# Kernel optimization log

Hardware: AMD Instinct MI355X
Metric: run time of the kernel (lower is better)

The kernel has to match this reference:

```python
import jax, jax.numpy as jnp
import numpy as np

N_NODES = 50000


def _segment_softmax(alpha, dst, num_segments):
    # alpha: [E, H] edge attention logits, softmax-normalized per destination node
    m = jax.ops.segment_max(alpha, dst, num_segments=num_segments)
    m = jnp.where(jnp.isfinite(m), m, 0.0)
    e = jnp.exp(alpha - m[dst])
    s = jax.ops.segment_sum(e, dst, num_segments=num_segments)
    return e / (s[dst] + 1e-16)


def _gat_layer(x, W, att_src, att_dst, bias, src, dst, heads, ch, concat):
    N = x.shape[0]
    xp = (x @ W).reshape(N, heads, ch)                      # [N, H, C]
    a_s = jnp.einsum('nhc,hc->nh', xp, att_src)              # [N, H]
    a_d = jnp.einsum('nhc,hc->nh', xp, att_dst)              # [N, H]
    alpha = jax.nn.leaky_relu(a_s[src] + a_d[dst], 0.2)      # [E, H]
    alpha = _segment_softmax(alpha, dst, N)
    out = jax.ops.segment_sum(alpha[:, :, None] * xp[src], dst, num_segments=N)  # [N, H, C]
    out = out.reshape(N, heads * ch) if concat else out.mean(axis=1)
    return out + bias


def setup_inputs() -> dict:
    key = jax.random.key(0)
    ks = jax.random.split(key, 10)
    IN, HID, HEADS, OUT, E = 128, 64, 4, 32, 640000
    x = jax.random.normal(ks[0], (N_NODES, IN), jnp.float32)
    edge_index = jax.random.randint(ks[1], (2, E), 0, N_NODES, dtype=jnp.int32)
    W1 = jax.random.normal(ks[2], (IN, HEADS * HID), jnp.float32) * (1.0 / np.sqrt(IN))
    att_src1 = jax.random.normal(ks[3], (HEADS, HID), jnp.float32) * 0.1
    att_dst1 = jax.random.normal(ks[4], (HEADS, HID), jnp.float32) * 0.1
    b1 = jnp.zeros((HEADS * HID,), jnp.float32)
    W2 = jax.random.normal(ks[5], (HEADS * HID, OUT), jnp.float32) * (1.0 / np.sqrt(HEADS * HID))
    att_src2 = jax.random.normal(ks[6], (1, OUT), jnp.float32) * 0.1
    att_dst2 = jax.random.normal(ks[7], (1, OUT), jnp.float32) * 0.1
    b2 = jnp.zeros((OUT,), jnp.float32)
    return {"x": x, "edge_index": edge_index, "W1": W1, "att_src1": att_src1,
            "att_dst1": att_dst1, "b1": b1, "W2": W2, "att_src2": att_src2,
            "att_dst2": att_dst2, "b2": b2}


def reference(x, edge_index, W1, att_src1, att_dst1, b1, W2, att_src2, att_dst2, b2):
    N = x.shape[0]
    # PyG GATConv default: add self-loops
    loop = jnp.arange(N, dtype=edge_index.dtype)
    src = jnp.concatenate([edge_index[0], loop])
    dst = jnp.concatenate([edge_index[1], loop])
    HID = att_src1.shape[1]
    HEADS = att_src1.shape[0]
    OUT = att_src2.shape[1]
    # dropout layers are identity in eval mode
    h = jax.nn.elu(_gat_layer(x, W1, att_src1, att_dst1, b1, src, dst, HEADS, HID, True))
    out = _gat_layer(h, W2, att_src2, att_dst2, b2, src, dst, 1, OUT, False)
    return jax.nn.softmax(out, axis=1)
```

## Files before the change

### kernel.cpp

```cpp
#include <hip/hip_runtime.h>
#include <math.h>
#include <stdint.h>

#define NEG_SENT -1e30f

typedef __attribute__((ext_vector_type(8))) short bf16x8;
typedef __attribute__((ext_vector_type(4))) float f32x4;

__device__ __forceinline__ unsigned short f2bf(float f) {
    unsigned u = __float_as_uint(f);
    unsigned r = u + 0x7FFFu + ((u >> 16) & 1u);
    return (unsigned short)(r >> 16);
}
__device__ __forceinline__ float bf2f(unsigned short h) {
    return __uint_as_float(((unsigned)h) << 16);
}

__global__ __launch_bounds__(256) void prep_count(const float* __restrict__ w1,
        const float* __restrict__ w2, unsigned short* __restrict__ w1t,
        unsigned short* __restrict__ w2t, const int* __restrict__ ei,
        int E, int Etot, int* __restrict__ deg) {
    int b = blockIdx.x;
    if (b < 160) {
        int tidx = b * 256 + threadIdx.x;
        if (b < 128) {
            int k = tidx & 127, n = tidx >> 7;
            w1t[tidx] = f2bf(w1[k * 256 + n]);
        } else {
            int idx = tidx - 32768;
            int k = idx & 255, n = idx >> 8;
            w2t[idx] = f2bf(w2[k * 32 + n]);
        }
    } else {
        int e = (b - 160) * 256 + threadIdx.x;
        if (e >= Etot) return;
        int d = (e < E) ? ei[E + e] : e - E;
        atomicAdd(&deg[d], 1);
    }
}

__global__ __launch_bounds__(256) void gemm1_mfma(
        const float* __restrict__ x,
        const unsigned short* __restrict__ w1t,
        const float* __restrict__ att_s, const float* __restrict__ att_d,
        unsigned short* __restrict__ xph,
        float* __restrict__ a_s, float* __restrict__ a_d, int M) {
    int wave = (int)(((long)blockIdx.x * 256 + threadIdx.x) >> 6);
    int lane = threadIdx.x & 63;
    int row0 = wave * 16;
    if (row0 >= M) return;
    int r = lane & 15;
    int g = lane >> 4;
    bf16x8 a[4];
    const float* arow = x + (long)(row0 + r) * 128 + g * 8;
    #pragma unroll
    for (int k0 = 0; k0 < 4; ++k0) {
        float4 f0 = *(const float4*)(arow + k0 * 32);
        float4 f1 = *(const float4*)(arow + k0 * 32 + 4);
        bf16x8 af;
        af[0] = (short)f2bf(f0.x); af[1] = (short)f2bf(f0.y);
        af[2] = (short)f2bf(f0.z); af[3] = (short)f2bf(f0.w);
        af[4] = (short)f2bf(f1.x); af[5] = (short)f2bf(f1.y);
        af[6] = (short)f2bf(f1.z); af[7] = (short)f2bf(f1.w);
        a[k0] = af;
    }
    float as_v[16], ad_v[16];
    #pragma unroll
    for (int nt = 0; nt < 16; ++nt) {
        as_v[nt] = att_s[nt * 16 + r];
        ad_v[nt] = att_d[nt * 16 + r];
    }
    f32x4 acc[16];
    #pragma unroll
    for (int nt = 0; nt < 16; ++nt) acc[nt] = (f32x4){0.f, 0.f, 0.f, 0.f};
    #pragma unroll
    for (int nt = 0; nt < 16; ++nt) {
        const unsigned short* brow = w1t + (long)(nt * 16 + r) * 128 + g * 8;
        #pragma unroll
        for (int k0 = 0; k0 < 4; ++k0) {
            bf16x8 b = *(const bf16x8*)(brow + k0 * 32);
            acc[nt] = __builtin_amdgcn_mfma_f32_16x16x32_bf16(a[k0], b, acc[nt], 0, 0, 0);
        }
    }
    float ps[4][4] = {};
    float pd[4][4] = {};
    #pragma unroll
    for (int nt = 0; nt < 16; ++nt) {
        int hh = nt >> 2;
        #pragma unroll
        for (int q = 0; q < 4; ++q) {
            float v = acc[nt][q];
            xph[(long)(row0 + g * 4 + q) * 256 + nt * 16 + r] = f2bf(v);
            ps[q][hh] += v * as_v[nt];
            pd[q][hh] += v * ad_v[nt];
        }
    }
    #pragma unroll
    for (int off = 1; off < 16; off <<= 1) {
        #pragma unroll
        for (int q = 0; q < 4; ++q)
            #pragma unroll
            for (int hh = 0; hh < 4; ++hh) {
                ps[q][hh] += __shfl_xor(ps[q][hh], off);
                pd[q][hh] += __shfl_xor(pd[q][hh], off);
            }
    }
    if (r == 0) {
        #pragma unroll
        for (int q = 0; q < 4; ++q) {
            int row = row0 + g * 4 + q;
            #pragma unroll
            for (int hh = 0; hh < 4; ++hh) {
                a_s[row * 4 + hh] = ps[q][hh];
                a_d[row * 4 + hh] = pd[q][hh];
            }
        }
    }
}

__global__ __launch_bounds__(256) void gemm2_mfma(
        const unsigned short* __restrict__ hb,
        const unsigned short* __restrict__ w2t,
        const float* __restrict__ att_s, const float* __restrict__ att_d,
        unsigned short* __restrict__ xp2h,
        float* __restrict__ a_s, float* __restrict__ a_d, int M) {
    int wave = (int)(((long)blockIdx.x * 256 + threadIdx.x) >> 6);
    int lane = threadIdx.x & 63;
    int row0 = wave * 16;
    if (row0 >= M) return;
    int r = lane & 15;
    int g = lane >> 4;
    bf16x8 a[8];
    const unsigned short* arow = hb + (long)(row0 + r) * 256 + g * 8;
    #pragma unroll
    for (int k0 = 0; k0 < 8; ++k0)
        a[k0] = *(const bf16x8*)(arow + k0 * 32);
    float as_v[2], ad_v[2];
    #pragma unroll
    for (int nt = 0; nt < 2; ++nt) {
        as_v[nt] = att_s[nt * 16 + r];
        ad_v[nt] = att_d[nt * 16 + r];
    }
    f32x4 acc[2];
    acc[0] = (f32x4){0.f, 0.f, 0.f, 0.f};
    acc[1] = (f32x4){0.f, 0.f, 0.f, 0.f};
    #pragma unroll
    for (int nt = 0; nt < 2; ++nt) {
        const unsigned short* brow = w2t + (long)(nt * 16 + r) * 256 + g * 8;
        #pragma unroll
        for (int k0 = 0; k0 < 8; ++k0) {
            bf16x8 b = *(const bf16x8*)(brow + k0 * 32);
            acc[nt] = __builtin_amdgcn_mfma_f32_16x16x32_bf16(a[k0], b, acc[nt], 0, 0, 0);
        }
    }
    float ps[4] = {}, pd[4] = {};
    #pragma unroll
    for (int nt = 0; nt < 2; ++nt) {
        #pragma unroll
        for (int q = 0; q < 4; ++q) {
            float v = acc[nt][q];
            xp2h[(long)(row0 + g * 4 + q) * 32 + nt * 16 + r] = f2bf(v);
            ps[q] += v * as_v[nt];
            pd[q] += v * ad_v[nt];
        }
    }
    #pragma unroll
    for (int off = 1; off < 16; off <<= 1) {
        #pragma unroll
        for (int q = 0; q < 4; ++q) {
            ps[q] += __shfl_xor(ps[q], off);
            pd[q] += __shfl_xor(pd[q], off);
        }
    }
    if (r == 0) {
        #pragma unroll
        for (int q = 0; q < 4; ++q) {
            a_s[row0 + g * 4 + q] = ps[q];
            a_d[row0 + g * 4 + q] = pd[q];
        }
    }
}

__global__ __launch_bounds__(256) void scan_local(const int* __restrict__ deg,
        int* __restrict__ rowptr, int* __restrict__ blocksum, int N) {
    __shared__ int part[256];
    int b = blockIdx.x, t = threadIdx.x;
    int base = b * 1024 + t * 4;
    int4 v = make_int4(0, 0, 0, 0);
    if (base + 3 < N) {
        v = *(const int4*)(deg + base);
    } else {
        if (base + 0 < N) v.x = deg[base + 0];
        if (base + 1 < N) v.y = deg[base + 1];
        if (base + 2 < N) v.z = deg[base + 2];
        if (base + 3 < N) v.w = deg[base + 3];
    }
    part[t] = v.x + v.y + v.z + v.w;
    __syncthreads();
    #pragma unroll
    for (int off = 1; off < 256; off <<= 1) {
        int val = (t >= off) ? part[t - off] : 0;
        __syncthreads();
        part[t] += val;
        __syncthreads();
    }
    if (t == 255) blocksum[b] = part[255];
    int r0 = (t > 0) ? part[t - 1] : 0;
    int r1 = r0 + v.x;
    int r2 = r1 + v.y;
    int r3 = r2 + v.z;
    if (base + 3 < N) {
        *(int4*)(rowptr + base) = make_int4(r0, r1, r2, r3);
    } else {
        if (base + 0 < N) rowptr[base + 0] = r0;
        if (base + 1 < N) rowptr[base + 1] = r1;
        if (base + 2 < N) rowptr[base + 2] = r2;
        if (base + 3 < N) rowptr[base + 3] = r3;
    }
}

__global__ __launch_bounds__(256) void scan_add(int* __restrict__ rowptr,
        const int* __restrict__ blocksum, int* __restrict__ cursor,
        int N, int Etot, int nb) {
    __shared__ int part[256];
    int b = blockIdx.x, t = threadIdx.x;
    part[t] = (t < nb) ? blocksum[t] : 0;
    __syncthreads();
    #pragma unroll
    for (int off = 1; off < 256; off <<= 1) {
        int val = (t >= off) ? part[t - off] : 0;
        __syncthreads();
        part[t] += val;
        __syncthreads();
    }
    int off_b = (b > 0) ? part[b - 1] : 0;
    int base = b * 1024 + t * 4;
    if (base + 3 < N) {
        int4 v = *(const int4*)(rowptr + base);
        v.x += off_b; v.y += off_b; v.z += off_b; v.w += off_b;
        *(int4*)(rowptr + base) = v;
        *(int4*)(cursor + base) = v;
    } else {
        for (int i = 0; i < 4; ++i) {
            if (base + i < N) {
                int v = rowptr[base + i] + off_b;
                rowptr[base + i] = v;
                cursor[base + i] = v;
            }
        }
    }
    if (b == 0 && t == 0) rowptr[N] = Etot;
}

__global__ __launch_bounds__(256) void scatter_edges(const int* __restrict__ ei,
        int E, int Etot, int* __restrict__ cursor, int* __restrict__ csr_src) {
    int e = blockIdx.x * 256 + threadIdx.x;
    if (e >= Etot) return;
    int s, d;
    if (e < E) { s = ei[e]; d = ei[E + e]; } else { s = e - E; d = s; }
    int pos = atomicAdd(&cursor[d], 1);
    csr_src[pos] = s;
}

__global__ __launch_bounds__(256) void sort_rows(const int* __restrict__ rowptr,
        int* __restrict__ csr_src, int N) {
    __shared__ int buf[4][256];
    int t = threadIdx.x;
    int w = t >> 6;
    int lane = t & 63;
    int d = blockIdx.x * 4 + w;
    if (d >= N) return;
    int row0 = rowptr[d];
    int deg = rowptr[d + 1] - row0;
    if (deg <= 64) {
        int v = (lane < deg) ? csr_src[row0 + lane] : 0x7FFFFFFF;
        #pragma unroll
        for (int k = 2; k <= 64; k <<= 1) {
            for (int jj = k >> 1; jj > 0; jj >>= 1) {
                int u = __shfl_xor(v, jj);
                bool up = ((lane & k) == 0);
                bool lower = ((lane & jj) == 0);
                int mn = min(v, u), mx = max(v, u);
                v = (up == lower) ? mn : mx;
            }
        }
        if (lane < deg) csr_src[row0 + lane] = v;
    } else if (deg <= 256) {
        for (int j = lane; j < deg; j += 64) buf[w][j] = csr_src[row0 + j];
        for (int it = 0; it < deg; ++it) {
            int start = it & 1;
            #pragma unroll
            for (int rep = 0; rep < 2; ++rep) {
                int k = start + 2 * lane + rep * 128;
                if (k + 1 < deg) {
                    int a = buf[w][k], b = buf[w][k + 1];
                    if (a > b) { buf[w][k] = b; buf[w][k + 1] = a; }
                }
            }
        }
        for (int j = lane; j < deg; j += 64) csr_src[row0 + j] = buf[w][j];
    } else if (lane == 0) {
        for (int i = 1; i < deg; ++i) {
            int key = csr_src[row0 + i];
            int k = i - 1;
            while (k >= 0 && csr_src[row0 + k] > key) {
                csr_src[row0 + k + 1] = csr_src[row0 + k];
                --k;
            }
            csr_src[row0 + k + 1] = key;
        }
    }
}

__global__ __launch_bounds__(256) void agg1_fused(const int* __restrict__ rowptr,
        const int* __restrict__ csr_src, const float* __restrict__ a_s,
        const float* __restrict__ a_d, const ushort4* __restrict__ xph4,
        const float* __restrict__ bias, ushort4* __restrict__ hb4, int N) {
    __shared__ unsigned short cbuf[4][1024];
    int t = threadIdx.x;
    int w = t >> 6;
    int lane = t & 63;
    int d = blockIdx.x * 4 + w;
    bool active = d < N;
    int row0 = 0, deg = 0;
    if (active) { row0 = rowptr[d]; deg = rowptr[d + 1] - row0; }
    int h = lane & 3;
    int j0 = lane >> 2;
    float ad = active ? a_d[d * 4 + h] : 0.f;
    float mraw = NEG_SENT;
    for (int j = j0; j < deg; j += 16) {
        int sn = csr_src[row0 + j];
        mraw = fmaxf(mraw, a_s[sn * 4 + h]);
    }
    #pragma unroll
    for (int off = 4; off <= 32; off <<= 1) mraw = fmaxf(mraw, __shfl_xor(mraw, off));
    float m = mraw + ad;
    m = m > 0.f ? m : 0.2f * m;
    float s = 0.f;
    for (int j = j0; j < deg; j += 16) {
        int sn = csr_src[row0 + j];
        float l = a_s[sn * 4 + h] + ad;
        l = l > 0.f ? l : 0.2f * l;
        float e = expf(l - m);
        if (j < 256) cbuf[w][j * 4 + h] = f2bf(e);
        s += e;
    }
    #pragma unroll
    for (int off = 4; off <= 32; off <<= 1) s += __shfl_xor(s, off);
    float inv = 1.f / (s + 1e-16f);
    if (!active) return;
    int hsel = lane >> 4;
    float m_h   = __shfl(m, hsel);
    float inv_h = __shfl(inv, hsel);
    float ad_h  = __shfl(ad, hsel);
    int cap = deg < 256 ? deg : 256;
    float4 acc = make_float4(0.f, 0.f, 0.f, 0.f);
    int j = 0;
    for (; j + 4 <= cap; j += 4) {
        long e0 = row0 + j;
        int s0 = csr_src[e0 + 0];
        int s1 = csr_src[e0 + 1];
        int s2 = csr_src[e0 + 2];
        int s3 = csr_src[e0 + 3];
        float c0 = bf2f(cbuf[w][(j + 0) * 4 + hsel]);
        float c1 = bf2f(cbuf[w][(j + 1) * 4 + hsel]);
        float c2 = bf2f(cbuf[w][(j + 2) * 4 + hsel]);
        float c3 = bf2f(cbuf[w][(j + 3) * 4 + hsel]);
        ushort4 u0 = xph4[(long)s0 * 64 + lane];
        ushort4 u1 = xph4[(long)s1 * 64 + lane];
        ushort4 u2 = xph4[(long)s2 * 64 + lane];
        ushort4 u3 = xph4[(long)s3 * 64 + lane];
        acc.x += c0 * bf2f(u0.x); acc.y += c0 * bf2f(u0.y);
        acc.z += c0 * bf2f(u0.z); acc.w += c0 * bf2f(u0.w);
        acc.x += c1 * bf2f(u1.x); acc.y += c1 * bf2f(u1.y);
        acc.z += c1 * bf2f(u1.z); acc.w += c1 * bf2f(u1.w);
        acc.x += c2 * bf2f(u2.x); acc.y += c2 * bf2f(u2.y);
        acc.z += c2 * bf2f(u2.z); acc.w += c2 * bf2f(u2.w);
        acc.x += c3 * bf2f(u3.x); acc.y += c3 * bf2f(u3.y);
        acc.z += c3 * bf2f(u3.z); acc.w += c3 * bf2f(u3.w);
    }
    for (; j < deg; ++j) {
        long e = row0 + j;
        int sn = csr_src[e];
        float c;
        if (j < 256) {
            c = bf2f(cbuf[w][j * 4 + hsel]);
        } else {
            float l = a_s[sn * 4 + hsel] + ad_h;
            l = l > 0.f ? l : 0.2f * l;
            c = bf2f(f2bf(expf(l - m_h)));
        }
        ushort4 u = xph4[(long)sn * 64 + lane];
        acc.x += c * bf2f(u.x); acc.y += c * bf2f(u.y);
        acc.z += c * bf2f(u.z); acc.w += c * bf2f(u.w);
    }
    float4 b = ((const float4*)bias)[lane];
    float vx = acc.x * inv_h + b.x; vx = vx > 0.f ? vx : expm1f(vx);
    float vy = acc.y * inv_h + b.y; vy = vy > 0.f ? vy : expm1f(vy);
    float vz = acc.z * inv_h + b.z; vz = vz > 0.f ? vz : expm1f(vz);
    float vw = acc.w * inv_h + b.w; vw = vw > 0.f ? vw : expm1f(vw);
    ushort4 o;
    o.x = f2bf(vx); o.y = f2bf(vy); o.z = f2bf(vz); o.w = f2bf(vw);
    hb4[(long)d * 64 + lane] = o;
}

__global__ __launch_bounds__(256) void agg2_fused(const int* __restrict__ rowptr,
        const int* __restrict__ csr_src, const float* __restrict__ a_s,
        const float* __restrict__ a_d, const unsigned short* __restrict__ xp2h,
        const float* __restrict__ bias, float* __restrict__ out, int N) {
    __shared__ unsigned short ebuf[8][256];
    int t = threadIdx.x;
    int w2 = t >> 5;
    int d = blockIdx.x * 8 + w2;
    if (d >= N) return;
    int c = t & 31;
    int row0 = rowptr[d];
    int deg = rowptr[d + 1] - row0;
    float ad = a_d[d];
    float mraw = NEG_SENT;
    for (int j = c; j < deg; j += 32) {
        int sn = csr_src[row0 + j];
        mraw = fmaxf(mraw, a_s[sn]);
    }
    #pragma unroll
    for (int off = 1; off <= 16; off <<= 1) mraw = fmaxf(mraw, __shfl_xor(mraw, off, 32));
    float m = mraw + ad;
    m = m > 0.f ? m : 0.2f * m;
    float s = 0.f;
    for (int j = c; j < deg; j += 32) {
        int sn = csr_src[row0 + j];
        float l = a_s[sn] + ad;
        l = l > 0.f ? l : 0.2f * l;
        float e = expf(l - m);
        if (j < 256) ebuf[w2][j] = f2bf(e);
        s += e;
    }
    #pragma unroll
    for (int off = 1; off <= 16; off <<= 1) s += __shfl_xor(s, off, 32);
    float inv = 1.f / (s + 1e-16f);
    int cap = deg < 256 ? deg : 256;
    float acc = 0.f;
    int j = 0;
    for (; j + 4 <= cap; j += 4) {
        long e0 = row0 + j;
        int s0 = csr_src[e0 + 0];
        int s1 = csr_src[e0 + 1];
        int s2 = csr_src[e0 + 2];
        int s3 = csr_src[e0 + 3];
        float c0 = bf2f(ebuf[w2][j + 0]);
        float c1 = bf2f(ebuf[w2][j + 1]);
        float c2 = bf2f(ebuf[w2][j + 2]);
        float c3 = bf2f(ebuf[w2][j + 3]);
        float v0 = bf2f(xp2h[(long)s0 * 32 + c]);
        float v1 = bf2f(xp2h[(long)s1 * 32 + c]);
        float v2 = bf2f(xp2h[(long)s2 * 32 + c]);
        float v3 = bf2f(xp2h[(long)s3 * 32 + c]);
        acc += c0 * v0;
        acc += c1 * v1;
        acc += c2 * v2;
        acc += c3 * v3;
    }
    for (; j < deg; ++j) {
        long e = row0 + j;
        int sn = csr_src[e];
        float co;
        if (j < 256) {
            co = bf2f(ebuf[w2][j]);
        } else {
            float l = a_s[sn] + ad; l = l > 0.f ? l : 0.2f * l;
            co = bf2f(f2bf(expf(l - m)));
        }
        acc += co * bf2f(xp2h[(long)sn * 32 + c]);
    }
    float v = acc * inv + bias[c];
    float mx = v;
    #pragma unroll
    for (int off = 16; off; off >>= 1) mx = fmaxf(mx, __shfl_xor(mx, off, 32));
    float ex = expf(v - mx);
    float sm = ex;
    #pragma unroll
    for (int off = 16; off; off >>= 1) sm += __shfl_xor(sm, off, 32);
    out[(long)d * 32 + c] = ex / sm;
}

extern "C" void kernel_launch(void* const* d_in, const int* in_sizes, int n_in,
                              void* d_out, int out_size, void* d_ws, size_t ws_size,
                              hipStream_t stream) {
    const float* x   = (const float*)d_in[0];
    const int*   ei  = (const int*)d_in[1];
    const float* W1  = (const float*)d_in[2];
    const float* as1 = (const float*)d_in[3];
    const float* ad1 = (const float*)d_in[4];
    const float* b1  = (const float*)d_in[5];
    const float* W2  = (const float*)d_in[6];
    const float* as2 = (const float*)d_in[7];
    const float* ad2 = (const float*)d_in[8];
    const float* b2  = (const float*)d_in[9];
    float* out = (float*)d_out;

    const int N = in_sizes[0] / 128;
    const int E = in_sizes[1] / 2;
    const int Etot = E + N;

    unsigned short* xp1h = (unsigned short*)d_ws;
    unsigned short* hb   = xp1h + (long)N * 256;
    unsigned short* w1t  = hb + (long)N * 256;
    unsigned short* w2t  = w1t + 32768;
    unsigned short* xp2h = w2t + 8192;
    float* a_s1   = (float*)(xp2h + (long)N * 32);
    float* a_d1   = a_s1 + (long)N * 4;
    float* a_s2   = a_d1 + (long)N * 4;
    float* a_d2   = a_s2 + N;
    int* deg      = (int*)(a_d2 + N);
    int* rowptr   = deg + N;
    int* cursor   = rowptr + N + 4;
    int* csr_src  = cursor + N;
    int* blocksum = csr_src + Etot;

    hipMemsetAsync(deg, 0, (size_t)N * sizeof(int), stream);

    int nbE = (Etot + 255) / 256;
    int nbS = (N + 1023) / 1024;
    prep_count<<<160 + nbE, 256, 0, stream>>>(W1, W2, w1t, w2t, ei, E, Etot, deg);
    scan_local<<<nbS, 256, 0, stream>>>(deg, rowptr, blocksum, N);
    scan_add<<<nbS, 256, 0, stream>>>(rowptr, blocksum, cursor, N, Etot, nbS);
    scatter_edges<<<nbE, 256, 0, stream>>>(ei, E, Etot, cursor, csr_src);
    sort_rows<<<(N + 3) / 4, 256, 0, stream>>>(rowptr, csr_src, N);

    int gemmBlocks = (((N + 15) / 16) + 3) / 4;

    gemm1_mfma<<<gemmBlocks, 256, 0, stream>>>(x, w1t, as1, ad1,
                                               xp1h, a_s1, a_d1, N);
    agg1_fused<<<(N + 3) / 4, 256, 0, stream>>>(rowptr, csr_src, a_s1, a_d1,
                                                (const ushort4*)xp1h, b1,
                                                (ushort4*)hb, N);

    gemm2_mfma<<<gemmBlocks, 256, 0, stream>>>(hb, w2t, as2, ad2,
                                               xp2h, a_s2, a_d2, N);
    agg2_fused<<<(N + 7) / 8, 256, 0, stream>>>(rowptr, csr_src, a_s2, a_d2,
                                                xp2h, b2, out, N);
}
```

Measured before the change: 235.3 us.

## Fuse per-row CSR sort into layer-1 aggregation and reuse sorted indices from registers

Removes the separate sort_rows kernel and sorts each destination row at the start of agg1_fused. The sorted result is still written back for agg2. For rows with degree up to 64, the sorted source indices stay in registers and are read with lane shuffles instead of being reloaded from global memory. This saves a launch and a full pass over csr_src, in exchange for a longer, more register-heavy aggregation kernel; an unused merge_ms helper is also added.

```diff
diff --git a/kernel.cpp b/kernel.cpp
--- a/kernel.cpp
+++ b/kernel.cpp
@@ -262,9 +262,18 @@
     csr_src[pos] = s;
 }
 
-__global__ __launch_bounds__(256) void sort_rows(const int* __restrict__ rowptr,
-        int* __restrict__ csr_src, int N) {
-    __shared__ int buf[4][256];
+__device__ __forceinline__ void merge_ms(float& m, float& s, float m2, float s2) {
+    float mn = fmaxf(m, m2);
+    s = s * expf(m - mn) + s2 * expf(m2 - mn);
+    m = mn;
+}
+
+__global__ __launch_bounds__(256) void agg1_fused(const int* __restrict__ rowptr,
+        int* __restrict__ csr_src, const float* __restrict__ a_s,
+        const float* __restrict__ a_d, const ushort4* __restrict__ xph4,
+        const float* __restrict__ bias, ushort4* __restrict__ hb4, int N) {
+    __shared__ int shmem[4][512];
+    unsigned short (*cbuf)[1024] = (unsigned short (*)[1024])shmem;
     int t = threadIdx.x;
     int w = t >> 6;
     int lane = t & 63;
@@ -272,33 +281,36 @@
     if (d >= N) return;
     int row0 = rowptr[d];
     int deg = rowptr[d + 1] - row0;
-    if (deg <= 64) {
-        int v = (lane < deg) ? csr_src[row0 + lane] : 0x7FFFFFFF;
+
+    int sv = 0x7FFFFFFF;
+    bool reg_sorted = (deg <= 64);
+    if (reg_sorted) {
+        if (lane < deg) sv = csr_src[row0 + lane];
         #pragma unroll
         for (int k = 2; k <= 64; k <<= 1) {
             for (int jj = k >> 1; jj > 0; jj >>= 1) {
-                int u = __shfl_xor(v, jj);
+                int u = __shfl_xor(sv, jj);
                 bool up = ((lane & k) == 0);
                 bool lower = ((lane & jj) == 0);
-                int mn = min(v, u), mx = max(v, u);
-                v = (up == lower) ? mn : mx;
+                int mn = min(sv, u), mx = max(sv, u);
+                sv = (up == lower) ? mn : mx;
             }
         }
-        if (lane < deg) csr_src[row0 + lane] = v;
+        if (lane < deg) csr_src[row0 + lane] = sv;
     } else if (deg <= 256) {
-        for (int j = lane; j < deg; j += 64) buf[w][j] = csr_src[row0 + j];
+        for (int j = lane; j < deg; j += 64) shmem[w][j] = csr_src[row0 + j];
         for (int it = 0; it < deg; ++it) {
             int start = it & 1;
             #pragma unroll
             for (int rep = 0; rep < 2; ++rep) {
                 int k = start + 2 * lane + rep * 128;
                 if (k + 1 < deg) {
-                    int a = buf[w][k], b = buf[w][k + 1];
-                    if (a > b) { buf[w][k] = b; buf[w][k + 1] = a; }
+                    int a = shmem[w][k], b = shmem[w][k + 1];
+                    if (a > b) { shmem[w][k] = b; shmem[w][k + 1] = a; }
                 }
             }
         }
-        for (int j = lane; j < deg; j += 64) csr_src[row0 + j] = buf[w][j];
+        for (int j = lane; j < deg; j += 64) csr_src[row0 + j] = shmem[w][j];
     } else if (lane == 0) {
         for (int i = 1; i < deg; ++i) {
             int key = csr_src[row0 + i];
@@ -310,45 +322,38 @@
             csr_src[row0 + k + 1] = key;
         }
     }
-}
-
-__global__ __launch_bounds__(256) void agg1_fused(const int* __restrict__ rowptr,
-        const int* __restrict__ csr_src, const float* __restrict__ a_s,
-        const float* __restrict__ a_d, const ushort4* __restrict__ xph4,
-        const float* __restrict__ bias, ushort4* __restrict__ hb4, int N) {
-    __shared__ unsigned short cbuf[4][1024];
-    int t = threadIdx.x;
-    int w = t >> 6;
-    int lane = t & 63;
-    int d = blockIdx.x * 4 + w;
-    bool active = d < N;
-    int row0 = 0, deg = 0;
-    if (active) { row0 = rowptr[d]; deg = rowptr[d + 1] - row0; }
+
     int h = lane & 3;
     int j0 = lane >> 2;
-    float ad = active ? a_d[d * 4 + h] : 0.f;
+    float ad = a_d[d * 4 + h];
+    int iters = (deg + 15) >> 4;
     float mraw = NEG_SENT;
-    for (int j = j0; j < deg; j += 16) {
-        int sn = csr_src[row0 + j];
-        mraw = fmaxf(mraw, a_s[sn * 4 + h]);
+    for (int it = 0; it < iters; ++it) {
+        int j = j0 + (it << 4);
+        int jc = (j < deg) ? j : 0;
+        int sn = reg_sorted ? __shfl(sv, jc) : csr_src[row0 + jc];
+        if (j < deg) mraw = fmaxf(mraw, a_s[sn * 4 + h]);
     }
     #pragma unroll
     for (int off = 4; off <= 32; off <<= 1) mraw = fmaxf(mraw, __shfl_xor(mraw, off));
     float m = mraw + ad;
     m = m > 0.f ? m : 0.2f * m;
     float s = 0.f;
-    for (int j = j0; j < deg; j += 16) {
-        int sn = csr_src[row0 + j];
-        float l = a_s[sn * 4 + h] + ad;
-        l = l > 0.f ? l : 0.2f * l;
-        float e = expf(l - m);
-        if (j < 256) cbuf[w][j * 4 + h] = f2bf(e);
-        s += e;
+    for (int it = 0; it < iters; ++it) {
+        int j = j0 + (it << 4);
+        int jc = (j < deg) ? j : 0;
+        int sn = reg_sorted ? __shfl(sv, jc) : csr_src[row0 + jc];
+        if (j < deg) {
+            float l = a_s[sn * 4 + h] + ad;
+            l = l > 0.f ? l : 0.2f * l;
+            float e = expf(l - m);
+            if (j < 256) cbuf[w][j * 4 + h] = f2bf(e);
+            s += e;
+        }
     }
     #pragma unroll
     for (int off = 4; off <= 32; off <<= 1) s += __shfl_xor(s, off);
     float inv = 1.f / (s + 1e-16f);
-    if (!active) return;
     int hsel = lane >> 4;
     float m_h   = __shfl(m, hsel);
     float inv_h = __shfl(inv, hsel);
@@ -357,11 +362,10 @@
     float4 acc = make_float4(0.f, 0.f, 0.f, 0.f);
     int j = 0;
     for (; j + 4 <= cap; j += 4) {
-        long e0 = row0 + j;
-        int s0 = csr_src[e0 + 0];
-        int s1 = csr_src[e0 + 1];
-        int s2 = csr_src[e0 + 2];
-        int s3 = csr_src[e0 + 3];
+        int s0 = reg_sorted ? __shfl(sv, j + 0) : csr_src[row0 + j + 0];
+        int s1 = reg_sorted ? __shfl(sv, j + 1) : csr_src[row0 + j + 1];
+        int s2 = reg_sorted ? __shfl(sv, j + 2) : csr_src[row0 + j + 2];
+        int s3 = reg_sorted ? __shfl(sv, j + 3) : csr_src[row0 + j + 3];
         float c0 = bf2f(cbuf[w][(j + 0) * 4 + hsel]);
         float c1 = bf2f(cbuf[w][(j + 1) * 4 + hsel]);
         float c2 = bf2f(cbuf[w][(j + 2) * 4 + hsel]);
@@ -380,8 +384,7 @@
         acc.z += c3 * bf2f(u3.z); acc.w += c3 * bf2f(u3.w);
     }
     for (; j < deg; ++j) {
-        long e = row0 + j;
-        int sn = csr_src[e];
+        int sn = reg_sorted ? __shfl(sv, j) : csr_src[row0 + j];
         float c;
         if (j < 256) {
             c = bf2f(cbuf[w][j * 4 + hsel]);
@@ -525,7 +528,6 @@
     scan_local<<<nbS, 256, 0, stream>>>(deg, rowptr, blocksum, N);
     scan_add<<<nbS, 256, 0, stream>>>(rowptr, blocksum, cursor, N, Etot, nbS);
     scatter_edges<<<nbE, 256, 0, stream>>>(ei, E, Etot, cursor, csr_src);
-    sort_rows<<<(N + 3) / 4, 256, 0, stream>>>(rowptr, csr_src, N);
 
     int gemmBlocks = (((N + 15) / 16) + 3) / 4;
 
```

After: 226.0 us (median of 2 runs). 1.04x faster.
